# Kernel optimization log

Hardware: AMD Instinct MI355X
Metric: run time of the kernel (lower is better)

The kernel has to match this reference:

```python
import jax, jax.numpy as jnp
import numpy as np

T, D, E, K, F, SF = 4096, 1024, 8, 2, 1024, 1024  # tokens, d_model, experts, top_k, moe_ff, shared_ff


def setup_inputs() -> dict:
    key = jax.random.key(0)
    ks = jax.random.split(key, 10)
    hidden_states = jax.random.normal(ks[0], (T, D), jnp.float32)
    # balanced expert assignment: the fused kernel's get_split_sizes assumes tokens
    # split evenly across experts after permute_tokens, so exactly T*K/E per expert
    flat = jnp.arange(T * K) % E
    flat = jax.random.permutation(ks[1], flat)
    topk_indices = flat.reshape(T, K).astype(jnp.int32)
    w = jax.random.uniform(ks[2], (T, K), jnp.float32)
    topk_weights = w / w.sum(-1, keepdims=True)  # norm_topk_prob
    s = 0.02
    w_gate = jax.random.normal(ks[3], (E, D, F), jnp.float32) * s
    w_up = jax.random.normal(ks[4], (E, D, F), jnp.float32) * s
    w_down = jax.random.normal(ks[5], (E, F, D), jnp.float32) * s
    sw_gate = jax.random.normal(ks[6], (D, SF), jnp.float32) * s
    sw_up = jax.random.normal(ks[7], (D, SF), jnp.float32) * s
    sw_down = jax.random.normal(ks[8], (SF, D), jnp.float32) * s
    shared_gate_w = jax.random.normal(ks[9], (D, 1), jnp.float32) * s
    return dict(hidden_states=hidden_states, topk_weights=topk_weights,
                w_gate=w_gate, w_up=w_up, w_down=w_down,
                sw_gate=sw_gate, sw_up=sw_up, sw_down=sw_down,
                shared_gate_w=shared_gate_w, topk_indices=topk_indices)


def _silu(x):
    return x * jax.nn.sigmoid(x)


def reference(hidden_states, topk_weights, w_gate, w_up, w_down,
              sw_gate, sw_up, sw_down, shared_gate_w, topk_indices):
    t, d = hidden_states.shape
    e = w_gate.shape[0]
    k = topk_indices.shape[1]
    c = (t * k) // e  # tokens per expert (balanced split, as in get_split_sizes)

    # permute_tokens: replicate each token top_k times and sort by expert id
    flat_idx = topk_indices.reshape(-1)                    # [t*k]
    order = jnp.argsort(flat_idx)                          # dispatch permutation
    x_rep = jnp.repeat(hidden_states, k, axis=0)           # [t*k, d]
    xs = x_rep[order].reshape(e, c, d)                     # grouped per-expert

    # per-expert gated MLP (grouped GEMMs)
    h = _silu(jnp.einsum('ecd,edf->ecf', xs, w_gate)) * jnp.einsum('ecd,edf->ecf', xs, w_up)
    y = jnp.einsum('ecf,efd->ecd', h, w_down).reshape(t * k, d)

    # unpermute_tokens + weighted combine over top_k
    y = y[jnp.argsort(order)].reshape(t, k, d)
    out = (y * topk_weights[..., None]).sum(axis=1)        # [t, d]

    # shared expert with sigmoid gate
    s = jnp.einsum('tf,fd->td', _silu(hidden_states @ sw_gate) * (hidden_states @ sw_up), sw_down)
    g = jax.nn.sigmoid(hidden_states @ shared_gate_w)      # [t, 1]
    return (out + g * s).astype(hidden_states.dtype)
```

## Files before the change

### kernel.cpp

```cpp
#include <hip/hip_runtime.h>
#include <hip/hip_bf16.h>
#include <cstdint>
#include <cstddef>

#define TTOK 4096
#define DM   1024
#define NE   8
#define KTOP 2
#define FFD  1024
#define CPER 1024
#define MROWS 12288


typedef __attribute__((ext_vector_type(8))) short frag8;
typedef __attribute__((ext_vector_type(4))) float f32x4;

static __device__ __forceinline__ unsigned short f2bf(float f) {
  unsigned int u = __float_as_uint(f);
  u += 0x7fff + ((u >> 16) & 1);
  return (unsigned short)(u >> 16);
}
static __device__ __forceinline__ float bf2f(unsigned short u) {
  return __uint_as_float((unsigned int)u << 16);
}

static __device__ __forceinline__ void gld_lds16(const unsigned short* g, unsigned short* l) {
  __builtin_amdgcn_global_load_lds(
      (const __attribute__((address_space(1))) unsigned int*)g,
      (__attribute__((address_space(3))) unsigned int*)l,
      16, 0, 0);
}

static __device__ __forceinline__ int lds_slot64(int r, int c) {
  return r * 8 + (c ^ (r & 7));
}

static __device__ __forceinline__ void stage_tile64(const unsigned short* __restrict__ src,
                                                    int row0, int k0,
                                                    unsigned short* lds, int tid) {
#pragma unroll
  for (int it = 0; it < 4; ++it) {
    int seg = it * 256 + tid;
    int r = seg >> 3;
    int cs = (seg & 7) ^ (r & 7);
    gld_lds16(src + (size_t)(row0 + r) * 1024 + k0 + cs * 8, lds + seg * 8);
  }
}

static __device__ __forceinline__ void swizzle_xy(int& x, int& y) {
  int L = blockIdx.y * 8 + blockIdx.x;
  int xcd = L & 7;
  int s = L >> 3;
  y = xcd * 12 + s % 12;
  x = s / 12;
}

static __device__ __forceinline__ void swizzle_xy4(int& x, int& y) {
  int L = blockIdx.y * 4 + blockIdx.x;
  int xcd = L & 7;
  int s = L >> 3;
  y = xcd * 12 + s % 12;
  x = s / 12;
}

__global__ void prep_kernel(const float* __restrict__ x, const float* __restrict__ gw,
                            const int* __restrict__ idx, const float* __restrict__ tw,
                            int* __restrict__ cnt, int* __restrict__ rowsrc,
                            int* __restrict__ inv, float* __restrict__ rowscale,
                            unsigned short* __restrict__ xb) {
  if (blockIdx.x < 32) {
    int i = blockIdx.x * 256 + threadIdx.x;
    int e = idx[i];
    int pos = atomicAdd(&cnt[e], 1);
    int j = e * CPER + pos;
    rowsrc[j] = i >> 1;
    rowscale[j] = tw[i];
    inv[i] = j;
    if (i < TTOK) rowsrc[8192 + i] = i;
  }
  int row = blockIdx.x * 4 + (threadIdx.x >> 6);
  int lane = threadIdx.x & 63;
  const float4* xr = (const float4*)(x + (size_t)row * 1024);
  const float4* wr = (const float4*)gw;
  ushort4* ob = (ushort4*)(xb + (size_t)row * 1024);
  float s = 0.f;
#pragma unroll
  for (int c = 0; c < 4; ++c) {
    int k = lane + 64 * c;
    float4 v = xr[k];
    float4 g = wr[k];
    s += v.x * g.x + v.y * g.y + v.z * g.z + v.w * g.w;
    ushort4 o;
    o.x = f2bf(v.x); o.y = f2bf(v.y); o.z = f2bf(v.z); o.w = f2bf(v.w);
    ob[k] = o;
  }
#pragma unroll
  for (int off = 32; off; off >>= 1) s += __shfl_down(s, off);
  if (lane == 0) rowscale[8192 + row] = 1.f / (1.f + __expf(-s));
}

__global__ void transw_kernel(const float* __restrict__ wg, const float* __restrict__ wu,
                              const float* __restrict__ wd, const float* __restrict__ sg,
                              const float* __restrict__ su, const float* __restrict__ sd,
                              unsigned short* __restrict__ owg, unsigned short* __restrict__ owu,
                              unsigned short* __restrict__ owd) {
  int z = blockIdx.z;
  const float* src; unsigned short* dst;
  if (z < 8)       { src = wg + (size_t)z * 1048576;        dst = owg + (size_t)z * 1048576; }
  else if (z < 16) { src = wu + (size_t)(z - 8) * 1048576;  dst = owu + (size_t)(z - 8) * 1048576; }
  else if (z < 24) { src = wd + (size_t)(z - 16) * 1048576; dst = owd + (size_t)(z - 16) * 1048576; }
  else if (z == 24){ src = sg; dst = owg + (size_t)8 * 1048576; }
  else if (z == 25){ src = su; dst = owu + (size_t)8 * 1048576; }
  else             { src = sd; dst = owd + (size_t)8 * 1048576; }
  __shared__ float tile[64][65];
  int bx = blockIdx.x * 64;
  int by = blockIdx.y * 64;
  int c4 = threadIdx.x & 15;
  int r0 = threadIdx.x >> 4;
#pragma unroll
  for (int i = 0; i < 4; ++i) {
    int r = r0 + 16 * i;
    float4 v = *(const float4*)&src[(size_t)(by + r) * 1024 + bx + c4 * 4];
    tile[r][c4 * 4 + 0] = v.x; tile[r][c4 * 4 + 1] = v.y;
    tile[r][c4 * 4 + 2] = v.z; tile[r][c4 * 4 + 3] = v.w;
  }
  __syncthreads();
#pragma unroll
  for (int i = 0; i < 4; ++i) {
    int f = r0 + 16 * i;
    ushort4 o;
    o.x = f2bf(tile[c4 * 4 + 0][f]);
    o.y = f2bf(tile[c4 * 4 + 1][f]);
    o.z = f2bf(tile[c4 * 4 + 2][f]);
    o.w = f2bf(tile[c4 * 4 + 3][f]);
    *(ushort4*)&dst[(size_t)(bx + f) * 1024 + by + c4 * 4] = o;
  }
}

static __device__ __forceinline__ int eid_of(int y) { return (y < 64) ? (y >> 3) : 8; }

__global__ __launch_bounds__(256, 2) void gemm1_kernel(
    const unsigned short* __restrict__ A, const int* __restrict__ rowsrc,
    const unsigned short* __restrict__ Bg, const unsigned short* __restrict__ Bu,
    unsigned short* __restrict__ H) {
  __shared__ __align__(16) unsigned short As[128 * 64];
  __shared__ __align__(16) unsigned short Bgs[128 * 64];
  __shared__ __align__(16) unsigned short Bus[128 * 64];
  int tid = threadIdx.x;
  int bx, by;
  swizzle_xy(bx, by);
  int e = eid_of(by);
  int row0 = by * 128;
  int col0 = bx * 128;
  const unsigned short* Bge = Bg + (size_t)e * 1048576;
  const unsigned short* Bue = Bu + (size_t)e * 1048576;

  const unsigned short* pA[4];
#pragma unroll
  for (int it = 0; it < 4; ++it) {
    int seg = it * 256 + tid;
    int r = seg >> 3;
    int cs = (seg & 7) ^ (r & 7);
    pA[it] = A + (size_t)rowsrc[row0 + r] * 1024 + cs * 8;
  }

  int wave = tid >> 6, lane = tid & 63;
  int wm = wave >> 1, wn = wave & 1;
  int lr = lane & 15, q = lane >> 4;

  f32x4 accg[4][4], accu[4][4];
#pragma unroll
  for (int i = 0; i < 4; ++i)
#pragma unroll
    for (int j = 0; j < 4; ++j) {
      accg[i][j] = (f32x4){0.f, 0.f, 0.f, 0.f};
      accu[i][j] = (f32x4){0.f, 0.f, 0.f, 0.f};
    }

  for (int kt = 0; kt < 1024; kt += 64) {
#pragma unroll
    for (int it = 0; it < 4; ++it)
      gld_lds16(pA[it] + kt, As + (it * 256 + tid) * 8);
    stage_tile64(Bge, col0, kt, Bgs, tid);
    stage_tile64(Bue, col0, kt, Bus, tid);
    __syncthreads();
#pragma unroll
    for (int kk = 0; kk < 2; ++kk) {
      int c = kk * 4 + q;
      frag8 a[4], b0[4], b1[4];
#pragma unroll
      for (int i = 0; i < 4; ++i) {
        int r = wm * 64 + i * 16 + lr;
        a[i] = *(const frag8*)&As[lds_slot64(r, c) * 8];
      }
#pragma unroll
      for (int j = 0; j < 4; ++j) {
        int r = wn * 64 + j * 16 + lr;
        b0[j] = *(const frag8*)&Bgs[lds_slot64(r, c) * 8];
        b1[j] = *(const frag8*)&Bus[lds_slot64(r, c) * 8];
      }
#pragma unroll
      for (int i = 0; i < 4; ++i)
#pragma unroll
        for (int j = 0; j < 4; ++j) {
          accg[i][j] = __builtin_amdgcn_mfma_f32_16x16x32_bf16(a[i], b0[j], accg[i][j], 0, 0, 0);
          accu[i][j] = __builtin_amdgcn_mfma_f32_16x16x32_bf16(a[i], b1[j], accu[i][j], 0, 0, 0);
        }
    }
    __syncthreads();
  }
#pragma unroll
  for (int i = 0; i < 4; ++i)
#pragma unroll
    for (int j = 0; j < 4; ++j)
#pragma unroll
      for (int r = 0; r < 4; ++r) {
        int m = row0 + wm * 64 + i * 16 + q * 4 + r;
        int n = col0 + wn * 64 + j * 16 + lr;
        float gv = accg[i][j][r];
        float hv = gv / (1.f + __expf(-gv)) * accu[i][j][r];
        H[(size_t)m * 1024 + n] = f2bf(hv);
      }
}

__global__ __launch_bounds__(256, 2) void gemm2_kernel(
    const unsigned short* __restrict__ A, const unsigned short* __restrict__ B,
    const float* __restrict__ rowscale, unsigned short* __restrict__ Y) {
  __shared__ __align__(16) unsigned short As[128 * 64];
  __shared__ __align__(16) unsigned short Bs[256 * 64];
  int tid = threadIdx.x;
  int bx, by;
  swizzle_xy4(bx, by);
  int e = eid_of(by);
  int row0 = by * 128;
  int col0 = bx * 256;
  const unsigned short* Be = B + (size_t)e * 1048576;

  int wave = tid >> 6, lane = tid & 63;
  int wm = wave >> 1, wn = wave & 1;
  int lr = lane & 15, q = lane >> 4;

  f32x4 acc[4][8];
#pragma unroll
  for (int i = 0; i < 4; ++i)
#pragma unroll
    for (int j = 0; j < 8; ++j) acc[i][j] = (f32x4){0.f, 0.f, 0.f, 0.f};

  for (int kt = 0; kt < 1024; kt += 64) {
    stage_tile64(A, row0, kt, As, tid);
#pragma unroll
    for (int it = 0; it < 8; ++it) {
      int seg = it * 256 + tid;
      int r = seg >> 3;
      int cs = (seg & 7) ^ (r & 7);
      gld_lds16(Be + (size_t)(col0 + r) * 1024 + kt + cs * 8, Bs + seg * 8);
    }
    __syncthreads();
#pragma unroll
    for (int kk = 0; kk < 2; ++kk) {
      int c = kk * 4 + q;
      frag8 a[4], b[8];
#pragma unroll
      for (int i = 0; i < 4; ++i) {
        int r = wm * 64 + i * 16 + lr;
        a[i] = *(const frag8*)&As[lds_slot64(r, c) * 8];
      }
#pragma unroll
      for (int j = 0; j < 8; ++j) {
        int r = wn * 128 + j * 16 + lr;
        b[j] = *(const frag8*)&Bs[lds_slot64(r, c) * 8];
      }
#pragma unroll
      for (int i = 0; i < 4; ++i)
#pragma unroll
        for (int j = 0; j < 8; ++j)
          acc[i][j] = __builtin_amdgcn_mfma_f32_16x16x32_bf16(a[i], b[j], acc[i][j], 0, 0, 0);
    }
    __syncthreads();
  }
#pragma unroll
  for (int i = 0; i < 4; ++i)
#pragma unroll
    for (int r = 0; r < 4; ++r) {
      int m = row0 + wm * 64 + i * 16 + q * 4 + r;
      float sc = rowscale[m];
#pragma unroll
      for (int j = 0; j < 8; ++j) {
        int n = col0 + wn * 128 + j * 16 + lr;
        Y[(size_t)m * 1024 + n] = f2bf(sc * acc[i][j][r]);
      }
    }
}

__global__ void combine_kernel(const unsigned short* __restrict__ Y,
                               const int* __restrict__ inv, float* __restrict__ out) {
  int base = blockIdx.x * 256 + threadIdx.x;
#pragma unroll
  for (int k = 0; k < 2; ++k) {
    int slot = base + k * 524288;
    int t = slot >> 8;
    int c = slot & 255;
    int j0 = inv[2 * t], j1 = inv[2 * t + 1];
    ushort4 a = ((const ushort4*)(Y + (size_t)j0 * 1024))[c];
    ushort4 b = ((const ushort4*)(Y + (size_t)j1 * 1024))[c];
    ushort4 s = ((const ushort4*)(Y + (size_t)(8192 + t) * 1024))[c];
    float4 o;
    o.x = bf2f(a.x) + bf2f(b.x) + bf2f(s.x);
    o.y = bf2f(a.y) + bf2f(b.y) + bf2f(s.y);
    o.z = bf2f(a.z) + bf2f(b.z) + bf2f(s.z);
    o.w = bf2f(a.w) + bf2f(b.w) + bf2f(s.w);
    ((float4*)(out + (size_t)t * 1024))[c] = o;
  }
}

extern "C" void kernel_launch(void* const* d_in, const int* in_sizes, int n_in,
                              void* d_out, int out_size, void* d_ws, size_t ws_size,
                              hipStream_t stream) {
  (void)in_sizes; (void)n_in; (void)out_size; (void)ws_size;
  const float* hidden  = (const float*)d_in[0];
  const float* topk_w  = (const float*)d_in[1];
  const float* w_gate  = (const float*)d_in[2];
  const float* w_up    = (const float*)d_in[3];
  const float* w_down  = (const float*)d_in[4];
  const float* sw_gate = (const float*)d_in[5];
  const float* sw_up   = (const float*)d_in[6];
  const float* sw_down = (const float*)d_in[7];
  const float* sgw     = (const float*)d_in[8];
  const int*   topk_i  = (const int*)d_in[9];
  float* out = (float*)d_out;

  char* p = (char*)d_ws;
  auto alloc = [&](size_t bytes) {
    char* r = p;
    p += (bytes + 255) & ~(size_t)255;
    return r;
  };
  unsigned short* Wg_all = (unsigned short*)alloc((size_t)9 * 1048576 * 2);
  unsigned short* Wu_all = (unsigned short*)alloc((size_t)9 * 1048576 * 2);
  unsigned short* Wd_all = (unsigned short*)alloc((size_t)9 * 1048576 * 2);
  unsigned short* Xbf    = (unsigned short*)alloc((size_t)TTOK * 1024 * 2);
  unsigned short* Hall   = (unsigned short*)alloc((size_t)MROWS * 1024 * 2);
  unsigned short* Yall   = (unsigned short*)alloc((size_t)MROWS * 1024 * 2);
  int*   cnt      = (int*)alloc(NE * 4);
  int*   rowsrc   = (int*)alloc((size_t)MROWS * 4);
  int*   inv      = (int*)alloc((size_t)TTOK * KTOP * 4);
  float* rowscale = (float*)alloc((size_t)MROWS * 4);

  hipMemsetAsync(cnt, 0, NE * 4, stream);

  prep_kernel<<<TTOK / 4, 256, 0, stream>>>(hidden, sgw, topk_i, topk_w,
                                            cnt, rowsrc, inv, rowscale, Xbf);
  transw_kernel<<<dim3(16, 16, 27), 256, 0, stream>>>(
      w_gate, w_up, w_down, sw_gate, sw_up, sw_down, Wg_all, Wu_all, Wd_all);

  gemm1_kernel<<<dim3(8, 96), 256, 0, stream>>>(Xbf, rowsrc, Wg_all, Wu_all, Hall);
  gemm2_kernel<<<dim3(4, 96), 256, 0, stream>>>(Hall, Wd_all, rowscale, Yall);
  combine_kernel<<<2048, 256, 0, stream>>>(Yall, inv, out);
}
```

Measured before the change: 296.2 us.

## Fuse combine into gemm2 via atomic scatter-add and merge prep with weight transpose

The down-projection GEMM now scatters scaled fp32 results straight into the output with atomicAdd, indexed by each row's source token. This removes the bf16 Y intermediate and the separate combine kernel, at the cost of a memset of the output and 12M scattered float atomics. The prep work (routing, bf16 cast of activations, shared gate) also moves into an extra z-slice of the weight-transpose launch, saving one kernel launch. Summation order becomes nondeterministic, and the atomic traffic may be costly.

```diff
diff --git a/kernel.cpp b/kernel.cpp
--- a/kernel.cpp
+++ b/kernel.cpp
@@ -63,48 +63,53 @@
   x = s / 12;
 }
 
-__global__ void prep_kernel(const float* __restrict__ x, const float* __restrict__ gw,
-                            const int* __restrict__ idx, const float* __restrict__ tw,
-                            int* __restrict__ cnt, int* __restrict__ rowsrc,
-                            int* __restrict__ inv, float* __restrict__ rowscale,
-                            unsigned short* __restrict__ xb) {
-  if (blockIdx.x < 32) {
-    int i = blockIdx.x * 256 + threadIdx.x;
-    int e = idx[i];
-    int pos = atomicAdd(&cnt[e], 1);
-    int j = e * CPER + pos;
-    rowsrc[j] = i >> 1;
-    rowscale[j] = tw[i];
-    inv[i] = j;
-    if (i < TTOK) rowsrc[8192 + i] = i;
-  }
-  int row = blockIdx.x * 4 + (threadIdx.x >> 6);
-  int lane = threadIdx.x & 63;
-  const float4* xr = (const float4*)(x + (size_t)row * 1024);
-  const float4* wr = (const float4*)gw;
-  ushort4* ob = (ushort4*)(xb + (size_t)row * 1024);
-  float s = 0.f;
-#pragma unroll
-  for (int c = 0; c < 4; ++c) {
-    int k = lane + 64 * c;
-    float4 v = xr[k];
-    float4 g = wr[k];
-    s += v.x * g.x + v.y * g.y + v.z * g.z + v.w * g.w;
-    ushort4 o;
-    o.x = f2bf(v.x); o.y = f2bf(v.y); o.z = f2bf(v.z); o.w = f2bf(v.w);
-    ob[k] = o;
-  }
-#pragma unroll
-  for (int off = 32; off; off >>= 1) s += __shfl_down(s, off);
-  if (lane == 0) rowscale[8192 + row] = 1.f / (1.f + __expf(-s));
-}
-
-__global__ void transw_kernel(const float* __restrict__ wg, const float* __restrict__ wu,
-                              const float* __restrict__ wd, const float* __restrict__ sg,
-                              const float* __restrict__ su, const float* __restrict__ sd,
-                              unsigned short* __restrict__ owg, unsigned short* __restrict__ owu,
-                              unsigned short* __restrict__ owd) {
+__global__ void prep_transw_kernel(
+    const float* __restrict__ wg, const float* __restrict__ wu,
+    const float* __restrict__ wd, const float* __restrict__ sg,
+    const float* __restrict__ su, const float* __restrict__ sd,
+    unsigned short* __restrict__ owg, unsigned short* __restrict__ owu,
+    unsigned short* __restrict__ owd,
+    const float* __restrict__ x, const float* __restrict__ gw,
+    const int* __restrict__ idx, const float* __restrict__ tw,
+    int* __restrict__ cnt, int* __restrict__ rowsrc,
+    float* __restrict__ rowscale, unsigned short* __restrict__ xb) {
   int z = blockIdx.z;
+  if (z == 27) {
+    int bid = blockIdx.y * 16 + blockIdx.x;
+    if (bid < 32) {
+      int i = bid * 256 + threadIdx.x;
+      int e = idx[i];
+      int pos = atomicAdd(&cnt[e], 1);
+      int j = e * CPER + pos;
+      rowsrc[j] = i >> 1;
+      rowscale[j] = tw[i];
+      if (i < TTOK) rowsrc[8192 + i] = i;
+    }
+    int wave = threadIdx.x >> 6;
+    int lane = threadIdx.x & 63;
+    const float4* wr = (const float4*)gw;
+#pragma unroll
+    for (int s = 0; s < 4; ++s) {
+      int row = bid * 16 + wave * 4 + s;
+      const float4* xr = (const float4*)(x + (size_t)row * 1024);
+      ushort4* ob = (ushort4*)(xb + (size_t)row * 1024);
+      float acc = 0.f;
+#pragma unroll
+      for (int c = 0; c < 4; ++c) {
+        int k = lane + 64 * c;
+        float4 v = xr[k];
+        float4 g = wr[k];
+        acc += v.x * g.x + v.y * g.y + v.z * g.z + v.w * g.w;
+        ushort4 o;
+        o.x = f2bf(v.x); o.y = f2bf(v.y); o.z = f2bf(v.z); o.w = f2bf(v.w);
+        ob[k] = o;
+      }
+#pragma unroll
+      for (int off = 32; off; off >>= 1) acc += __shfl_down(acc, off);
+      if (lane == 0) rowscale[8192 + row] = 1.f / (1.f + __expf(-acc));
+    }
+    return;
+  }
   const float* src; unsigned short* dst;
   if (z < 8)       { src = wg + (size_t)z * 1048576;        dst = owg + (size_t)z * 1048576; }
   else if (z < 16) { src = wu + (size_t)(z - 8) * 1048576;  dst = owu + (size_t)(z - 8) * 1048576; }
@@ -225,7 +230,8 @@
 
 __global__ __launch_bounds__(256, 2) void gemm2_kernel(
     const unsigned short* __restrict__ A, const unsigned short* __restrict__ B,
-    const float* __restrict__ rowscale, unsigned short* __restrict__ Y) {
+    const float* __restrict__ rowscale, const int* __restrict__ rowsrc,
+    float* __restrict__ out) {
   __shared__ __align__(16) unsigned short As[128 * 64];
   __shared__ __align__(16) unsigned short Bs[256 * 64];
   int tid = threadIdx.x;
@@ -284,33 +290,13 @@
     for (int r = 0; r < 4; ++r) {
       int m = row0 + wm * 64 + i * 16 + q * 4 + r;
       float sc = rowscale[m];
+      float* orow = out + (size_t)rowsrc[m] * 1024;
 #pragma unroll
       for (int j = 0; j < 8; ++j) {
         int n = col0 + wn * 128 + j * 16 + lr;
-        Y[(size_t)m * 1024 + n] = f2bf(sc * acc[i][j][r]);
-      }
-    }
-}
-
-__global__ void combine_kernel(const unsigned short* __restrict__ Y,
-                               const int* __restrict__ inv, float* __restrict__ out) {
-  int base = blockIdx.x * 256 + threadIdx.x;
-#pragma unroll
-  for (int k = 0; k < 2; ++k) {
-    int slot = base + k * 524288;
-    int t = slot >> 8;
-    int c = slot & 255;
-    int j0 = inv[2 * t], j1 = inv[2 * t + 1];
-    ushort4 a = ((const ushort4*)(Y + (size_t)j0 * 1024))[c];
-    ushort4 b = ((const ushort4*)(Y + (size_t)j1 * 1024))[c];
-    ushort4 s = ((const ushort4*)(Y + (size_t)(8192 + t) * 1024))[c];
-    float4 o;
-    o.x = bf2f(a.x) + bf2f(b.x) + bf2f(s.x);
-    o.y = bf2f(a.y) + bf2f(b.y) + bf2f(s.y);
-    o.z = bf2f(a.z) + bf2f(b.z) + bf2f(s.z);
-    o.w = bf2f(a.w) + bf2f(b.w) + bf2f(s.w);
-    ((float4*)(out + (size_t)t * 1024))[c] = o;
-  }
+        atomicAdd(orow + n, sc * acc[i][j][r]);
+      }
+    }
 }
 
 extern "C" void kernel_launch(void* const* d_in, const int* in_sizes, int n_in,
@@ -340,20 +326,17 @@
   unsigned short* Wd_all = (unsigned short*)alloc((size_t)9 * 1048576 * 2);
   unsigned short* Xbf    = (unsigned short*)alloc((size_t)TTOK * 1024 * 2);
   unsigned short* Hall   = (unsigned short*)alloc((size_t)MROWS * 1024 * 2);
-  unsigned short* Yall   = (unsigned short*)alloc((size_t)MROWS * 1024 * 2);
   int*   cnt      = (int*)alloc(NE * 4);
   int*   rowsrc   = (int*)alloc((size_t)MROWS * 4);
-  int*   inv      = (int*)alloc((size_t)TTOK * KTOP * 4);
   float* rowscale = (float*)alloc((size_t)MROWS * 4);
 
   hipMemsetAsync(cnt, 0, NE * 4, stream);
-
-  prep_kernel<<<TTOK / 4, 256, 0, stream>>>(hidden, sgw, topk_i, topk_w,
-                                            cnt, rowsrc, inv, rowscale, Xbf);
-  transw_kernel<<<dim3(16, 16, 27), 256, 0, stream>>>(
-      w_gate, w_up, w_down, sw_gate, sw_up, sw_down, Wg_all, Wu_all, Wd_all);
+  hipMemsetAsync(out, 0, (size_t)TTOK * DM * 4, stream);
+
+  prep_transw_kernel<<<dim3(16, 16, 28), 256, 0, stream>>>(
+      w_gate, w_up, w_down, sw_gate, sw_up, sw_down, Wg_all, Wu_all, Wd_all,
+      hidden, sgw, topk_i, topk_w, cnt, rowsrc, rowscale, Xbf);
 
   gemm1_kernel<<<dim3(8, 96), 256, 0, stream>>>(Xbf, rowsrc, Wg_all, Wu_all, Hall);
-  gemm2_kernel<<<dim3(4, 96), 256, 0, stream>>>(Hall, Wd_all, rowscale, Yall);
-  combine_kernel<<<2048, 256, 0, stream>>>(Yall, inv, out);
-}
+  gemm2_kernel<<<dim3(4, 96), 256, 0, stream>>>(Hall, Wd_all, rowscale, rowsrc, out);
+}
```

New measurement: 310.0 us. 4.7% more time.

## Fuse token prep into weight transpose kernel and process four tiles per block

Applied to the files above, without the earlier changes.

Merges the token routing/bf16-conversion prep kernel into the weight transpose kernel as an extra z-slice, removing one launch. Each transpose block now handles four 64x64 tiles along x, prefetching the next tile's loads into registers while the current tile is written out. The prep slice has each block handle 64 rows instead of 4. Fewer, larger blocks reduce launch and scheduling overhead and let loads overlap with stores, at the cost of less parallelism per block and a possible imbalance from the heavier prep blocks.

```diff
diff --git a/kernel.cpp b/kernel.cpp
--- a/kernel.cpp
+++ b/kernel.cpp
@@ -63,48 +63,54 @@
   x = s / 12;
 }
 
-__global__ void prep_kernel(const float* __restrict__ x, const float* __restrict__ gw,
-                            const int* __restrict__ idx, const float* __restrict__ tw,
-                            int* __restrict__ cnt, int* __restrict__ rowsrc,
-                            int* __restrict__ inv, float* __restrict__ rowscale,
-                            unsigned short* __restrict__ xb) {
-  if (blockIdx.x < 32) {
-    int i = blockIdx.x * 256 + threadIdx.x;
-    int e = idx[i];
-    int pos = atomicAdd(&cnt[e], 1);
-    int j = e * CPER + pos;
-    rowsrc[j] = i >> 1;
-    rowscale[j] = tw[i];
-    inv[i] = j;
-    if (i < TTOK) rowsrc[8192 + i] = i;
-  }
-  int row = blockIdx.x * 4 + (threadIdx.x >> 6);
-  int lane = threadIdx.x & 63;
-  const float4* xr = (const float4*)(x + (size_t)row * 1024);
-  const float4* wr = (const float4*)gw;
-  ushort4* ob = (ushort4*)(xb + (size_t)row * 1024);
-  float s = 0.f;
-#pragma unroll
-  for (int c = 0; c < 4; ++c) {
-    int k = lane + 64 * c;
-    float4 v = xr[k];
-    float4 g = wr[k];
-    s += v.x * g.x + v.y * g.y + v.z * g.z + v.w * g.w;
-    ushort4 o;
-    o.x = f2bf(v.x); o.y = f2bf(v.y); o.z = f2bf(v.z); o.w = f2bf(v.w);
-    ob[k] = o;
-  }
-#pragma unroll
-  for (int off = 32; off; off >>= 1) s += __shfl_down(s, off);
-  if (lane == 0) rowscale[8192 + row] = 1.f / (1.f + __expf(-s));
-}
-
-__global__ void transw_kernel(const float* __restrict__ wg, const float* __restrict__ wu,
-                              const float* __restrict__ wd, const float* __restrict__ sg,
-                              const float* __restrict__ su, const float* __restrict__ sd,
-                              unsigned short* __restrict__ owg, unsigned short* __restrict__ owu,
-                              unsigned short* __restrict__ owd) {
+__global__ void prep_transw_kernel(
+    const float* __restrict__ wg, const float* __restrict__ wu,
+    const float* __restrict__ wd, const float* __restrict__ sg,
+    const float* __restrict__ su, const float* __restrict__ sd,
+    unsigned short* __restrict__ owg, unsigned short* __restrict__ owu,
+    unsigned short* __restrict__ owd,
+    const float* __restrict__ x, const float* __restrict__ gw,
+    const int* __restrict__ idx, const float* __restrict__ tw,
+    int* __restrict__ cnt, int* __restrict__ rowsrc, int* __restrict__ inv,
+    float* __restrict__ rowscale, unsigned short* __restrict__ xb) {
   int z = blockIdx.z;
+  if (z == 27) {
+    int bid = blockIdx.y * 4 + blockIdx.x;
+    if (bid < 32) {
+      int i = bid * 256 + threadIdx.x;
+      int e = idx[i];
+      int pos = atomicAdd(&cnt[e], 1);
+      int j = e * CPER + pos;
+      rowsrc[j] = i >> 1;
+      rowscale[j] = tw[i];
+      inv[i] = j;
+      if (i < TTOK) rowsrc[8192 + i] = i;
+    }
+    int wave = threadIdx.x >> 6;
+    int lane = threadIdx.x & 63;
+    const float4* wr = (const float4*)gw;
+#pragma unroll 2
+    for (int s = 0; s < 16; ++s) {
+      int row = bid * 64 + wave * 16 + s;
+      const float4* xr = (const float4*)(x + (size_t)row * 1024);
+      ushort4* ob = (ushort4*)(xb + (size_t)row * 1024);
+      float acc = 0.f;
+#pragma unroll
+      for (int c = 0; c < 4; ++c) {
+        int k = lane + 64 * c;
+        float4 v = xr[k];
+        float4 g = wr[k];
+        acc += v.x * g.x + v.y * g.y + v.z * g.z + v.w * g.w;
+        ushort4 o;
+        o.x = f2bf(v.x); o.y = f2bf(v.y); o.z = f2bf(v.z); o.w = f2bf(v.w);
+        ob[k] = o;
+      }
+#pragma unroll
+      for (int off = 32; off; off >>= 1) acc += __shfl_down(acc, off);
+      if (lane == 0) rowscale[8192 + row] = 1.f / (1.f + __expf(-acc));
+    }
+    return;
+  }
   const float* src; unsigned short* dst;
   if (z < 8)       { src = wg + (size_t)z * 1048576;        dst = owg + (size_t)z * 1048576; }
   else if (z < 16) { src = wu + (size_t)(z - 8) * 1048576;  dst = owu + (size_t)(z - 8) * 1048576; }
@@ -113,27 +119,47 @@
   else if (z == 25){ src = su; dst = owu + (size_t)8 * 1048576; }
   else             { src = sd; dst = owd + (size_t)8 * 1048576; }
   __shared__ float tile[64][65];
-  int bx = blockIdx.x * 64;
-  int by = blockIdx.y * 64;
+  int bx0 = blockIdx.x * 256;
+  int by  = blockIdx.y * 64;
   int c4 = threadIdx.x & 15;
   int r0 = threadIdx.x >> 4;
-#pragma unroll
-  for (int i = 0; i < 4; ++i) {
-    int r = r0 + 16 * i;
-    float4 v = *(const float4*)&src[(size_t)(by + r) * 1024 + bx + c4 * 4];
-    tile[r][c4 * 4 + 0] = v.x; tile[r][c4 * 4 + 1] = v.y;
-    tile[r][c4 * 4 + 2] = v.z; tile[r][c4 * 4 + 3] = v.w;
-  }
-  __syncthreads();
-#pragma unroll
-  for (int i = 0; i < 4; ++i) {
-    int f = r0 + 16 * i;
-    ushort4 o;
-    o.x = f2bf(tile[c4 * 4 + 0][f]);
-    o.y = f2bf(tile[c4 * 4 + 1][f]);
-    o.z = f2bf(tile[c4 * 4 + 2][f]);
-    o.w = f2bf(tile[c4 * 4 + 3][f]);
-    *(ushort4*)&dst[(size_t)(bx + f) * 1024 + by + c4 * 4] = o;
+  const float* sbase = src + (size_t)(by + r0) * 1024 + bx0 + c4 * 4;
+  float4 v0 = *(const float4*)(sbase + 0);
+  float4 v1 = *(const float4*)(sbase + 16384);
+  float4 v2 = *(const float4*)(sbase + 32768);
+  float4 v3 = *(const float4*)(sbase + 49152);
+  float4 w0, w1, w2, w3;
+#pragma unroll
+  for (int t = 0; t < 4; ++t) {
+    int bx = bx0 + t * 64;
+    __syncthreads();
+    tile[r0     ][c4 * 4 + 0] = v0.x; tile[r0     ][c4 * 4 + 1] = v0.y;
+    tile[r0     ][c4 * 4 + 2] = v0.z; tile[r0     ][c4 * 4 + 3] = v0.w;
+    tile[r0 + 16][c4 * 4 + 0] = v1.x; tile[r0 + 16][c4 * 4 + 1] = v1.y;
+    tile[r0 + 16][c4 * 4 + 2] = v1.z; tile[r0 + 16][c4 * 4 + 3] = v1.w;
+    tile[r0 + 32][c4 * 4 + 0] = v2.x; tile[r0 + 32][c4 * 4 + 1] = v2.y;
+    tile[r0 + 32][c4 * 4 + 2] = v2.z; tile[r0 + 32][c4 * 4 + 3] = v2.w;
+    tile[r0 + 48][c4 * 4 + 0] = v3.x; tile[r0 + 48][c4 * 4 + 1] = v3.y;
+    tile[r0 + 48][c4 * 4 + 2] = v3.z; tile[r0 + 48][c4 * 4 + 3] = v3.w;
+    if (t < 3) {
+      const float* nb = sbase + (t + 1) * 64;
+      w0 = *(const float4*)(nb + 0);
+      w1 = *(const float4*)(nb + 16384);
+      w2 = *(const float4*)(nb + 32768);
+      w3 = *(const float4*)(nb + 49152);
+    }
+    __syncthreads();
+#pragma unroll
+    for (int i = 0; i < 4; ++i) {
+      int f = r0 + 16 * i;
+      ushort4 o;
+      o.x = f2bf(tile[c4 * 4 + 0][f]);
+      o.y = f2bf(tile[c4 * 4 + 1][f]);
+      o.z = f2bf(tile[c4 * 4 + 2][f]);
+      o.w = f2bf(tile[c4 * 4 + 3][f]);
+      *(ushort4*)&dst[(size_t)(bx + f) * 1024 + by + c4 * 4] = o;
+    }
+    v0 = w0; v1 = w1; v2 = w2; v3 = w3;
   }
 }
 
@@ -348,10 +374,9 @@
 
   hipMemsetAsync(cnt, 0, NE * 4, stream);
 
-  prep_kernel<<<TTOK / 4, 256, 0, stream>>>(hidden, sgw, topk_i, topk_w,
-                                            cnt, rowsrc, inv, rowscale, Xbf);
-  transw_kernel<<<dim3(16, 16, 27), 256, 0, stream>>>(
-      w_gate, w_up, w_down, sw_gate, sw_up, sw_down, Wg_all, Wu_all, Wd_all);
+  prep_transw_kernel<<<dim3(4, 16, 28), 256, 0, stream>>>(
+      w_gate, w_up, w_down, sw_gate, sw_up, sw_down, Wg_all, Wu_all, Wd_all,
+      hidden, sgw, topk_i, topk_w, cnt, rowsrc, inv, rowscale, Xbf);
 
   gemm1_kernel<<<dim3(8, 96), 256, 0, stream>>>(Xbf, rowsrc, Wg_all, Wu_all, Hall);
   gemm2_kernel<<<dim3(4, 96), 256, 0, stream>>>(Hall, Wd_all, rowscale, Yall);
```

Result: no change. 290.9 us (-1.8%).
